# Kernel tuning notes

Hardware: AMD Instinct MI355X
Metric: run time of the kernel (lower is better)

## Reference

```python
import jax, jax.numpy as jnp
import numpy as np

N_QUBITS = 16
BATCH = 256


def _apply_1q(state, gate, wire, n):
    # state: (B, 2**n) complex64; gate: (2,2) shared or (B,2,2) per-sample.
    # PennyLane default.qubit: wire 0 is the most-significant bit.
    B = state.shape[0]
    s = state.reshape(B, 2 ** wire, 2, 2 ** (n - wire - 1))
    if gate.ndim == 3:
        s = jnp.einsum('bij,bljr->blir', gate, s)
    else:
        s = jnp.einsum('ij,bljr->blir', gate, s)
    return s.reshape(B, -1)


def _cnot(state, ctrl, n):
    # CNOT with control=ctrl, target=ctrl+1 (adjacent wires).
    B = state.shape[0]
    s = state.reshape(B, 2 ** ctrl, 2, 2, 2 ** (n - ctrl - 2))
    s = s.at[:, :, 1].set(s[:, :, 1, ::-1])  # flip target where control==1
    return s.reshape(B, -1)


def _ry(theta):
    # theta: (B,) -> (B,2,2) complex64
    c = jnp.cos(theta / 2).astype(jnp.complex64)
    s = jnp.sin(theta / 2).astype(jnp.complex64)
    return jnp.stack([jnp.stack([c, -s], -1), jnp.stack([s, c], -1)], -2)


def _rz(theta):
    # theta: scalar -> (2,2) complex64, diag(e^{-i t/2}, e^{+i t/2})
    e = jnp.exp(-0.5j * theta.astype(jnp.complex64))
    z = jnp.zeros((), jnp.complex64)
    return jnp.stack([jnp.stack([e, z]), jnp.stack([z, jnp.conj(e)])])


def _rx(theta):
    c = jnp.cos(theta / 2).astype(jnp.complex64)
    s = (-1j * jnp.sin(theta / 2)).astype(jnp.complex64)
    return jnp.stack([jnp.stack([c, s]), jnp.stack([s, c])])


def _circuit(x, params, n):
    # x: (B, n) float angles (already padded/truncated to n qubits)
    B = x.shape[0]
    state = jnp.zeros((B, 2 ** n), jnp.complex64).at[:, 0].set(1.0)
    for _ in range(3):
        for i in range(n):
            state = _apply_1q(state, _ry(x[:, i] * jnp.pi), i, n)
        for i in range(n):
            state = _apply_1q(state, _rz(params[i, 0]), i, n)
            state = _apply_1q(state, _rx(params[i, 1]), i, n)
        for i in range(n - 1):
            state = _cnot(state, i, n)
    return state


def setup_inputs() -> dict:
    key = jax.random.key(0)
    k1, k2 = jax.random.split(key)
    x = jax.random.uniform(k1, (BATCH, N_QUBITS), dtype=jnp.float32)
    params = 0.1 * jax.random.normal(k2, (N_QUBITS, 2), dtype=jnp.float32)
    return {"x": x, "params": params}


def reference(x, params):
    n = params.shape[0]
    f = x.shape[1]
    if f < n:
        x = jnp.pad(x, ((0, 0), (0, n - f)))
    elif f > n:
        x = x[:, :n]
    return _circuit(x, params, n)
```

## Files before the change

### kernel.cpp

```cpp
#include <hip/hip_runtime.h>
#include <stdint.h>

#define PI_F 3.14159265358979323846f

__device__ __forceinline__ float2 cmul(float2 a, float2 b) {
    return make_float2(fmaf(a.x, b.x, -a.y * b.y),
                       fmaf(a.x, b.y,  a.y * b.x));
}
__device__ __forceinline__ float2 cfma(float2 a, float2 b, float2 c) {
    return make_float2(fmaf(a.x, b.x, fmaf(-a.y, b.y, c.x)),
                       fmaf(a.x, b.y, fmaf( a.y, b.x, c.y)));
}

__device__ __forceinline__ uint32_t pack_c(float2 v) {
    uint32_t a = __float_as_uint(v.x), b = __float_as_uint(v.y);
    a = (a + 0x7FFFu + ((a >> 16) & 1u)) >> 16;
    b = (b + 0x7FFFu + ((b >> 16) & 1u)) >> 16;
    return a | (b << 16);
}
__device__ __forceinline__ uint32_t pack_fin(float2 v) {
    uint32_t a = __float_as_uint(v.x), b = __float_as_uint(v.y);
    a = (a + 0x7FFFu + ((a >> 16) & 1u)) >> 16;
    b = (b + 0x7FFFu + ((b >> 16) & 1u)) >> 16;
    return b | (a << 16);
}
__device__ __forceinline__ float2 unpack_c(uint32_t u) {
    return make_float2(__uint_as_float(u << 16), __uint_as_float(u & 0xFFFF0000u));
}

__device__ __forceinline__ int g5(int v)  { return (v ^ (v >> 1)) & 31; }
__device__ __forceinline__ int ig5(int v) { v ^= v >> 1; v ^= v >> 2; v ^= v >> 4; return v & 31; }
__device__ __forceinline__ int ig6(int v) { v ^= v >> 1; v ^= v >> 2; v ^= v >> 4; return v & 63; }

#define LDC(w, idx) make_float2(sU[(w)*8 + (idx)*2], sU[(w)*8 + (idx)*2 + 1])
#define FCOL(w, beta) make_float2(sU[(w)*8 + (beta)*4], sU[(w)*8 + (beta)*4 + 1])

__device__ __forceinline__ void build_table(float* sU, const float* __restrict__ x,
                                            const float* __restrict__ par, int batch, int tid) {
    if (tid < 16) {
        const int w = tid;
        float sy, cy, sz, cz, sx, cx;
        sincosf(0.5f * PI_F * x[batch * 16 + w], &sy, &cy);
        sincosf(0.5f * par[w * 2 + 0], &sz, &cz);
        sincosf(0.5f * par[w * 2 + 1], &sx, &cx);
        float ccc = cx * cy * cz, sss = sx * sy * sz;
        float ccs = cx * cy * sz, ssc = sx * sy * cz;
        float csc = cx * sy * cz, scs = sx * cy * sz;
        float css = cx * sy * sz, scc = sx * cy * cz;
        float* o = sU + w * 8;
        o[0] = ccc + sss;  o[1] = -(ccs + ssc);
        o[2] = scs - csc;  o[3] = css - scc;
        o[4] = csc - scs;  o[5] = css - scc;
        o[6] = ccc + sss;  o[7] = ccs + ssc;
    }
    __syncthreads();
}

__device__ __forceinline__ void apply11_T(float2 (&A)[32], const float* __restrict__ sU, int lane) {
    #pragma unroll
    for (int p = 0; p <= 5; ++p) {
        const int w = 15 - p;
        float2 u00 = LDC(w, 0), u01 = LDC(w, 1), u10 = LDC(w, 2), u11 = LDC(w, 3);
        const int myb = (lane >> p) & 1;
        float2 ca = myb ? u11 : u00;
        float2 cb = myb ? u10 : u01;
        #pragma unroll
        for (int r = 0; r < 32; ++r) {
            float px = __shfl_xor(A[r].x, 1 << p, 64);
            float py = __shfl_xor(A[r].y, 1 << p, 64);
            A[r] = cfma(cb, make_float2(px, py), cmul(ca, A[r]));
        }
    }
    #pragma unroll
    for (int k = 0; k <= 4; ++k) {
        const int w = 9 - k;
        float2 u00 = LDC(w, 0), u01 = LDC(w, 1), u10 = LDC(w, 2), u11 = LDC(w, 3);
        const int m = 1 << k;
        #pragma unroll
        for (int g = 0; g < 16; ++g) {
            int i = ((g >> k) << (k + 1)) | (g & (m - 1));
            int j = i | m;
            float2 a = A[i], b = A[j];
            A[i] = cfma(u01, b, cmul(u00, a));
            A[j] = cfma(u11, b, cmul(u10, a));
        }
    }
}

__global__ __launch_bounds__(256, 4) void k_pass1(const float* __restrict__ x,
                                                  const float* __restrict__ par,
                                                  uint32_t* __restrict__ out) {
    __shared__ float sU[128];
    const int tid = threadIdx.x, lane = tid & 63, wv = tid >> 6;
    const int L = ((blockIdx.x & 7) << 8) | (blockIdx.x >> 3);
    const int batch = L >> 3;
    build_table(sU, x, par, batch, tid);
    const int chunk = ((L & 7) << 2) | wv;

    const int gc = chunk ^ (chunk >> 1);
    float2 com = make_float2(1.f, 0.f);
    #pragma unroll
    for (int p = 11; p <= 15; ++p)
        com = cmul(com, FCOL(15 - p, (gc >> (p - 11)) & 1));
    #pragma unroll
    for (int p = 0; p <= 4; ++p)
        com = cmul(com, FCOL(15 - p, ((lane >> p) ^ (lane >> (p + 1))) & 1));

    const int l5 = (lane >> 5) & 1;
    const int c0 = chunk & 1;
    const float2 fa10 = FCOL(10, l5), fb10 = FCOL(10, l5 ^ 1);
    const float2 fa9  = FCOL(9, 0),   fb9  = FCOL(9, 1);
    const float2 fa8  = FCOL(8, 0),   fb8  = FCOL(8, 1);
    const float2 fa7  = FCOL(7, 0),   fb7  = FCOL(7, 1);
    const float2 fa6  = FCOL(6, 0),   fb6  = FCOL(6, 1);
    const float2 fa5  = FCOL(5, c0),  fb5  = FCOL(5, c0 ^ 1);
    float2 A[32];
    #pragma unroll
    for (int r = 0; r < 32; ++r) {
        float2 v = com;
        v = cmul(v, ((r & 1) != 0)                     ? fb10 : fa10);
        v = cmul(v, ((((r >> 0) ^ (r >> 1)) & 1) != 0) ? fb9 : fa9);
        v = cmul(v, ((((r >> 1) ^ (r >> 2)) & 1) != 0) ? fb8 : fa8);
        v = cmul(v, ((((r >> 2) ^ (r >> 3)) & 1) != 0) ? fb7 : fa7);
        v = cmul(v, ((((r >> 3) ^ (r >> 4)) & 1) != 0) ? fb6 : fa6);
        v = cmul(v, (((r >> 4) & 1) != 0)              ? fb5 : fa5);
        A[r] = v;
    }
    apply11_T(A, sU, lane);
    uint32_t* base = out + (((size_t)batch << 16) | (chunk << 11));
    const int igl = ig6(lane);
    #pragma unroll
    for (int r = 0; r < 32; ++r) {
        const int addr = (ig5(r) << 6) | (igl ^ ((__popc(r) & 1) ? 63 : 0));
        base[addr] = pack_c(A[r]);
    }
}

__global__ __launch_bounds__(256, 2) void k_pass2(const float* __restrict__ x,
                                                  const float* __restrict__ par,
                                                  uint32_t* __restrict__ out) {
    __shared__ float sU[128];
    const int tid = threadIdx.x;
    const int L = ((blockIdx.x & 7) << 7) | (blockIdx.x >> 3);
    const int batch = L >> 2;
    build_table(sU, x, par, batch, tid);
    const int y = ((L & 3) << 8) | tid;
    uint32_t* base = out + ((size_t)batch << 16);

    float2 A[2][32];
    #pragma unroll
    for (int t = 0; t < 32; ++t)
        #pragma unroll
        for (int d = 0; d < 2; ++d)
            A[d][t] = unpack_c(base[(t << 11) | (d << 10) | (y ^ (d ? 1023 : 0))]);

    #pragma unroll
    for (int j = 0; j < 5; ++j) {
        const int w = 4 - j, m = 1 << j;
        float2 u00 = LDC(w, 0), u01 = LDC(w, 1), u10 = LDC(w, 2), u11 = LDC(w, 3);
        #pragma unroll
        for (int d = 0; d < 2; ++d)
        #pragma unroll
        for (int g = 0; g < 16; ++g) {
            int t0 = ((g >> j) << (j + 1)) | (g & (m - 1));
            int t1 = t0 | m;
            float2 a = A[d][t0], b = A[d][t1];
            A[d][t0] = cfma(u01, b, cmul(u00, a));
            A[d][t1] = cfma(u11, b, cmul(u10, a));
        }
    }
    #pragma unroll
    for (int k = 0; k < 5; ++k) {
        const int w = 4 - k, m = 1 << k;
        float2 u00 = LDC(w, 0), u01 = LDC(w, 1), u10 = LDC(w, 2), u11 = LDC(w, 3);
        #pragma unroll
        for (int mu = 0; mu < 2; ++mu)
        #pragma unroll
        for (int q = 0; q < 16; ++q) {
            int h0 = ((q >> k) << (k + 1)) | (q & (m - 1));
            int h1 = h0 | m;
            const int dA = (mu ^ (h0 & 1)) & 1, rA = g5(h0);
            const int dB = (mu ^ (h1 & 1)) & 1, rB = g5(h1);
            float2 a = A[dA][rA], b = A[dB][rB];
            A[dA][rA] = cfma(u01, b, cmul(u00, a));
            A[dB][rB] = cfma(u11, b, cmul(u10, a));
        }
    }
    asm volatile("s_waitcnt vmcnt(0)" ::: "memory");
    #pragma unroll
    for (int h = 0; h < 32; ++h) {
        const int sl = ig5(h);
        #pragma unroll
        for (int mu = 0; mu < 2; ++mu)
            base[(sl << 11) | (mu << 10) | (y ^ (mu ? 1023 : 0))] =
                pack_c(A[(mu ^ (h & 1)) & 1][g5(h)]);
    }
}

__global__ __launch_bounds__(256, 4) void k_pass3(const float* __restrict__ x,
                                                  const float* __restrict__ par,
                                                  uint32_t* __restrict__ out) {
    __shared__ float sU[128];
    const int tid = threadIdx.x, lane = tid & 63, wv = tid >> 6;
    const int L = ((blockIdx.x & 7) << 8) | (blockIdx.x >> 3);
    const int batch = L >> 3;
    build_table(sU, x, par, batch, tid);
    const int v = ((L & 7) << 2) | wv;
    uint32_t* sb = out + (((size_t)batch << 16) | (v << 11));
    float2 A[32];
    #pragma unroll
    for (int r = 0; r < 32; ++r)
        A[r] = unpack_c(sb[(r << 6) | lane]);
    apply11_T(A, sU, lane);
    asm volatile("s_waitcnt vmcnt(0)" ::: "memory");
    const int cmask = (v & 1) ? 0x7FF : 0;
    const int igl = ig6(lane);
    #pragma unroll
    for (int r = 0; r < 32; ++r) {
        const int addr = ((ig5(r) << 6) | (igl ^ ((__popc(r) & 1) ? 63 : 0))) ^ cmask;
        __builtin_nontemporal_store(pack_fin(A[r]), &sb[addr]);
    }
}

extern "C" void kernel_launch(void* const* d_in, const int* in_sizes, int n_in,
                              void* d_out, int out_size, void* d_ws, size_t ws_size,
                              hipStream_t stream) {
    const float* x   = (const float*)d_in[0];
    const float* par = (const float*)d_in[1];
    if (n_in >= 2 && in_sizes[0] < in_sizes[1]) {
        x   = (const float*)d_in[1];
        par = (const float*)d_in[0];
    }
    uint32_t* out = (uint32_t*)d_out;
    const dim3 blk(256);
    hipLaunchKernelGGL(k_pass1, dim3(2048), blk, 0, stream, x, par, out);
    hipLaunchKernelGGL(k_pass2, dim3(1024), blk, 0, stream, x, par, out);
    hipLaunchKernelGGL(k_pass3, dim3(2048), blk, 0, stream, x, par, out);
}
```

Baseline: 190.2 us.

## Fuse three global-memory passes into one per-batch kernel using LDS exchange

Replaces the three kernels, which round-trip the bf16-packed state through global memory, with one kernel that launches a 1024-thread block per batch sample. Two half-state steps pass data through a 128 KB LDS buffer, and the transposition that pass 2 did via global memory now happens in registers and LDS. This removes two full global write/read round trips and two launches. In exchange, each block uses a large LDS allocation, the grid is only 256 blocks with heavy register pressure, and extra __syncthreads barriers are added. Requantizing state to bf16 between the pass-2 phases also changes where rounding occurs.

```diff
diff --git a/kernel.cpp b/kernel.cpp
--- a/kernel.cpp
+++ b/kernel.cpp
@@ -87,138 +87,152 @@
     }
 }
 
-__global__ __launch_bounds__(256, 4) void k_pass1(const float* __restrict__ x,
-                                                  const float* __restrict__ par,
-                                                  uint32_t* __restrict__ out) {
+__global__ __launch_bounds__(1024, 4) void k_fused(const float* __restrict__ x,
+                                                   const float* __restrict__ par,
+                                                   uint32_t* __restrict__ out) {
     __shared__ float sU[128];
+    __shared__ uint32_t ex[32768];
     const int tid = threadIdx.x, lane = tid & 63, wv = tid >> 6;
-    const int L = ((blockIdx.x & 7) << 8) | (blockIdx.x >> 3);
-    const int batch = L >> 3;
+    const int batch = blockIdx.x;
     build_table(sU, x, par, batch, tid);
-    const int chunk = ((L & 7) << 2) | wv;
-
-    const int gc = chunk ^ (chunk >> 1);
-    float2 com = make_float2(1.f, 0.f);
-    #pragma unroll
-    for (int p = 11; p <= 15; ++p)
-        com = cmul(com, FCOL(15 - p, (gc >> (p - 11)) & 1));
-    #pragma unroll
-    for (int p = 0; p <= 4; ++p)
-        com = cmul(com, FCOL(15 - p, ((lane >> p) ^ (lane >> (p + 1))) & 1));
-
-    const int l5 = (lane >> 5) & 1;
-    const int c0 = chunk & 1;
-    const float2 fa10 = FCOL(10, l5), fb10 = FCOL(10, l5 ^ 1);
-    const float2 fa9  = FCOL(9, 0),   fb9  = FCOL(9, 1);
-    const float2 fa8  = FCOL(8, 0),   fb8  = FCOL(8, 1);
-    const float2 fa7  = FCOL(7, 0),   fb7  = FCOL(7, 1);
-    const float2 fa6  = FCOL(6, 0),   fb6  = FCOL(6, 1);
-    const float2 fa5  = FCOL(5, c0),  fb5  = FCOL(5, c0 ^ 1);
-    float2 A[32];
-    #pragma unroll
-    for (int r = 0; r < 32; ++r) {
-        float2 v = com;
-        v = cmul(v, ((r & 1) != 0)                     ? fb10 : fa10);
-        v = cmul(v, ((((r >> 0) ^ (r >> 1)) & 1) != 0) ? fb9 : fa9);
-        v = cmul(v, ((((r >> 1) ^ (r >> 2)) & 1) != 0) ? fb8 : fa8);
-        v = cmul(v, ((((r >> 2) ^ (r >> 3)) & 1) != 0) ? fb7 : fa7);
-        v = cmul(v, ((((r >> 3) ^ (r >> 4)) & 1) != 0) ? fb6 : fa6);
-        v = cmul(v, (((r >> 4) & 1) != 0)              ? fb5 : fa5);
-        A[r] = v;
-    }
-    apply11_T(A, sU, lane);
-    uint32_t* base = out + (((size_t)batch << 16) | (chunk << 11));
-    const int igl = ig6(lane);
-    #pragma unroll
-    for (int r = 0; r < 32; ++r) {
-        const int addr = (ig5(r) << 6) | (igl ^ ((__popc(r) & 1) ? 63 : 0));
-        base[addr] = pack_c(A[r]);
-    }
-}
-
-__global__ __launch_bounds__(256, 2) void k_pass2(const float* __restrict__ x,
-                                                  const float* __restrict__ par,
-                                                  uint32_t* __restrict__ out) {
-    __shared__ float sU[128];
-    const int tid = threadIdx.x;
-    const int L = ((blockIdx.x & 7) << 7) | (blockIdx.x >> 3);
-    const int batch = L >> 2;
-    build_table(sU, x, par, batch, tid);
-    const int y = ((L & 3) << 8) | tid;
-    uint32_t* base = out + ((size_t)batch << 16);
-
-    float2 A[2][32];
-    #pragma unroll
-    for (int t = 0; t < 32; ++t)
-        #pragma unroll
-        for (int d = 0; d < 2; ++d)
-            A[d][t] = unpack_c(base[(t << 11) | (d << 10) | (y ^ (d ? 1023 : 0))]);
-
-    #pragma unroll
-    for (int j = 0; j < 5; ++j) {
-        const int w = 4 - j, m = 1 << j;
-        float2 u00 = LDC(w, 0), u01 = LDC(w, 1), u10 = LDC(w, 2), u11 = LDC(w, 3);
-        #pragma unroll
-        for (int d = 0; d < 2; ++d)
-        #pragma unroll
-        for (int g = 0; g < 16; ++g) {
-            int t0 = ((g >> j) << (j + 1)) | (g & (m - 1));
-            int t1 = t0 | m;
-            float2 a = A[d][t0], b = A[d][t1];
-            A[d][t0] = cfma(u01, b, cmul(u00, a));
-            A[d][t1] = cfma(u11, b, cmul(u10, a));
-        }
-    }
-    #pragma unroll
-    for (int k = 0; k < 5; ++k) {
-        const int w = 4 - k, m = 1 << k;
-        float2 u00 = LDC(w, 0), u01 = LDC(w, 1), u10 = LDC(w, 2), u11 = LDC(w, 3);
+
+    uint32_t P[2][32];
+
+    #pragma unroll
+    for (int step = 0; step < 2; ++step) {
+        const int chunk = wv | (step << 4);
+        const int gc = chunk ^ (chunk >> 1);
+        float2 com = make_float2(1.f, 0.f);
+        #pragma unroll
+        for (int p = 11; p <= 15; ++p)
+            com = cmul(com, FCOL(15 - p, (gc >> (p - 11)) & 1));
+        #pragma unroll
+        for (int p = 0; p <= 4; ++p)
+            com = cmul(com, FCOL(15 - p, ((lane >> p) ^ (lane >> (p + 1))) & 1));
+        const int l5 = (lane >> 5) & 1;
+        const int c0 = chunk & 1;
+        const float2 fa10 = FCOL(10, l5), fb10 = FCOL(10, l5 ^ 1);
+        const float2 fa9  = FCOL(9, 0),   fb9  = FCOL(9, 1);
+        const float2 fa8  = FCOL(8, 0),   fb8  = FCOL(8, 1);
+        const float2 fa7  = FCOL(7, 0),   fb7  = FCOL(7, 1);
+        const float2 fa6  = FCOL(6, 0),   fb6  = FCOL(6, 1);
+        const float2 fa5  = FCOL(5, c0),  fb5  = FCOL(5, c0 ^ 1);
+        float2 A[32];
+        #pragma unroll
+        for (int r = 0; r < 32; ++r) {
+            float2 v = com;
+            v = cmul(v, ((r & 1) != 0)                     ? fb10 : fa10);
+            v = cmul(v, ((((r >> 0) ^ (r >> 1)) & 1) != 0) ? fb9 : fa9);
+            v = cmul(v, ((((r >> 1) ^ (r >> 2)) & 1) != 0) ? fb8 : fa8);
+            v = cmul(v, ((((r >> 2) ^ (r >> 3)) & 1) != 0) ? fb7 : fa7);
+            v = cmul(v, ((((r >> 3) ^ (r >> 4)) & 1) != 0) ? fb6 : fa6);
+            v = cmul(v, (((r >> 4) & 1) != 0)              ? fb5 : fa5);
+            A[r] = v;
+        }
+        apply11_T(A, sU, lane);
+        {
+            uint32_t* lb = ex + ((chunk & 15) << 11);
+            const int igl = ig6(lane);
+            #pragma unroll
+            for (int r = 0; r < 32; ++r)
+                lb[(ig5(r) << 6) | (igl ^ ((__popc(r) & 1) ? 63 : 0))] = pack_c(A[r]);
+        }
+        __syncthreads();
+        #pragma unroll
+        for (int tt = 0; tt < 16; ++tt) {
+            #pragma unroll
+            for (int d = 0; d < 2; ++d)
+                P[d][(step << 4) | tt] =
+                    ex[(tt << 11) | (d << 10) | (tid ^ (d ? 1023 : 0))];
+        }
+        __syncthreads();
+    }
+
+    #pragma unroll
+    for (int d = 0; d < 2; ++d) {
+        float2 B[32];
+        #pragma unroll
+        for (int t = 0; t < 32; ++t) B[t] = unpack_c(P[d][t]);
+        #pragma unroll
+        for (int j = 0; j < 5; ++j) {
+            const int w = 4 - j, m = 1 << j;
+            float2 u00 = LDC(w, 0), u01 = LDC(w, 1), u10 = LDC(w, 2), u11 = LDC(w, 3);
+            #pragma unroll
+            for (int g = 0; g < 16; ++g) {
+                const int t0 = ((g >> j) << (j + 1)) | (g & (m - 1));
+                const int t1 = t0 | m;
+                float2 a = B[t0], b = B[t1];
+                B[t0] = cfma(u01, b, cmul(u00, a));
+                B[t1] = cfma(u11, b, cmul(u10, a));
+            }
+        }
+        #pragma unroll
+        for (int t = 0; t < 32; ++t) P[d][t] = pack_c(B[t]);
+    }
+    {
+        float2 u00 = LDC(4, 0), u01 = LDC(4, 1), u10 = LDC(4, 2), u11 = LDC(4, 3);
         #pragma unroll
         for (int mu = 0; mu < 2; ++mu)
         #pragma unroll
         for (int q = 0; q < 16; ++q) {
-            int h0 = ((q >> k) << (k + 1)) | (q & (m - 1));
-            int h1 = h0 | m;
-            const int dA = (mu ^ (h0 & 1)) & 1, rA = g5(h0);
-            const int dB = (mu ^ (h1 & 1)) & 1, rB = g5(h1);
-            float2 a = A[dA][rA], b = A[dB][rB];
-            A[dA][rA] = cfma(u01, b, cmul(u00, a));
-            A[dB][rB] = cfma(u11, b, cmul(u10, a));
-        }
-    }
-    asm volatile("s_waitcnt vmcnt(0)" ::: "memory");
-    #pragma unroll
-    for (int h = 0; h < 32; ++h) {
-        const int sl = ig5(h);
-        #pragma unroll
-        for (int mu = 0; mu < 2; ++mu)
-            base[(sl << 11) | (mu << 10) | (y ^ (mu ? 1023 : 0))] =
-                pack_c(A[(mu ^ (h & 1)) & 1][g5(h)]);
-    }
-}
-
-__global__ __launch_bounds__(256, 4) void k_pass3(const float* __restrict__ x,
-                                                  const float* __restrict__ par,
-                                                  uint32_t* __restrict__ out) {
-    __shared__ float sU[128];
-    const int tid = threadIdx.x, lane = tid & 63, wv = tid >> 6;
-    const int L = ((blockIdx.x & 7) << 8) | (blockIdx.x >> 3);
-    const int batch = L >> 3;
-    build_table(sU, x, par, batch, tid);
-    const int v = ((L & 7) << 2) | wv;
-    uint32_t* sb = out + (((size_t)batch << 16) | (v << 11));
-    float2 A[32];
-    #pragma unroll
-    for (int r = 0; r < 32; ++r)
-        A[r] = unpack_c(sb[(r << 6) | lane]);
-    apply11_T(A, sU, lane);
-    asm volatile("s_waitcnt vmcnt(0)" ::: "memory");
-    const int cmask = (v & 1) ? 0x7FF : 0;
-    const int igl = ig6(lane);
-    #pragma unroll
-    for (int r = 0; r < 32; ++r) {
-        const int addr = ((ig5(r) << 6) | (igl ^ ((__popc(r) & 1) ? 63 : 0))) ^ cmask;
-        __builtin_nontemporal_store(pack_fin(A[r]), &sb[addr]);
+            const int h0 = 2 * q, h1 = 2 * q + 1;
+            const int dA = mu, dB = mu ^ 1;
+            const int rA = g5(h0), rB = g5(h1);
+            float2 a = unpack_c(P[dA][rA]), b = unpack_c(P[dB][rB]);
+            P[dA][rA] = pack_c(cfma(u01, b, cmul(u00, a)));
+            P[dB][rB] = pack_c(cfma(u11, b, cmul(u10, a)));
+        }
+    }
+    #pragma unroll
+    for (int d = 0; d < 2; ++d) {
+        float2 B[32];
+        #pragma unroll
+        for (int t = 0; t < 32; ++t) B[t] = unpack_c(P[d][t]);
+        #pragma unroll
+        for (int k = 1; k < 5; ++k) {
+            const int w = 4 - k, m = 1 << k;
+            float2 u00 = LDC(w, 0), u01 = LDC(w, 1), u10 = LDC(w, 2), u11 = LDC(w, 3);
+            #pragma unroll
+            for (int q = 0; q < 16; ++q) {
+                const int h0 = ((q >> k) << (k + 1)) | (q & (m - 1));
+                const int h1 = h0 | m;
+                const int rA = g5(h0), rB = g5(h1);
+                float2 a = B[rA], b = B[rB];
+                B[rA] = cfma(u01, b, cmul(u00, a));
+                B[rB] = cfma(u11, b, cmul(u10, a));
+            }
+        }
+        #pragma unroll
+        for (int t = 0; t < 32; ++t) P[d][t] = pack_c(B[t]);
+    }
+
+    #pragma unroll
+    for (int step = 0; step < 2; ++step) {
+        #pragma unroll
+        for (int hh = 0; hh < 16; ++hh) {
+            const int h = (step << 4) | hh;
+            const int sl = ig5(h) & 15;
+            #pragma unroll
+            for (int mu = 0; mu < 2; ++mu)
+                ex[(sl << 11) | (mu << 10) | (tid ^ (mu ? 1023 : 0))] =
+                    P[(mu ^ (h & 1)) & 1][g5(h)];
+        }
+        __syncthreads();
+        const int v = wv | (step << 4);
+        float2 A[32];
+        #pragma unroll
+        for (int r = 0; r < 32; ++r)
+            A[r] = unpack_c(ex[((v & 15) << 11) | (r << 6) | lane]);
+        apply11_T(A, sU, lane);
+        uint32_t* sb = out + (((size_t)batch << 16) | (v << 11));
+        const int cmask = (v & 1) ? 0x7FF : 0;
+        const int igl = ig6(lane);
+        #pragma unroll
+        for (int r = 0; r < 32; ++r) {
+            const int addr = ((ig5(r) << 6) | (igl ^ ((__popc(r) & 1) ? 63 : 0))) ^ cmask;
+            __builtin_nontemporal_store(pack_fin(A[r]), &sb[addr]);
+        }
+        __syncthreads();
     }
 }
 
@@ -232,8 +246,5 @@
         par = (const float*)d_in[0];
     }
     uint32_t* out = (uint32_t*)d_out;
-    const dim3 blk(256);
-    hipLaunchKernelGGL(k_pass1, dim3(2048), blk, 0, stream, x, par, out);
-    hipLaunchKernelGGL(k_pass2, dim3(1024), blk, 0, stream, x, par, out);
-    hipLaunchKernelGGL(k_pass3, dim3(2048), blk, 0, stream, x, par, out);
-}
+    hipLaunchKernelGGL(k_fused, dim3(256), dim3(1024), 0, stream, x, par, out);
+}
```

Result: no change. 189.5 us (-0.4%).
